# Kernel optimization log

Measured on AMD Instinct MI355X. Metric: run time of the kernel, lower is better.

The kernel has to match this reference:

```python
import jax, jax.numpy as jnp
import numpy as np

B, N1, N2, F = 8, 256, 256, 128


def setup_inputs() -> dict:
    key = jax.random.key(0)
    ks = jax.random.split(key, 12)
    s = 1.0 / np.sqrt(F)
    return {
        "x1": jax.random.normal(ks[0], (B, N1, F), jnp.float32),
        "x2": jax.random.normal(ks[1], (B, N2, F), jnp.float32),
        "valid_edge": (jax.random.uniform(ks[2], (B, N1, N2)) < 0.2).astype(jnp.float32),
        "W_w": jax.random.uniform(ks[3], (F, F), jnp.float32, -s, s),
        "W_b": jax.random.uniform(ks[4], (F,), jnp.float32, -s, s),
        "M_w": jax.random.uniform(ks[5], (F, F), jnp.float32, -s, s),
        "M_b": jax.random.uniform(ks[6], (F,), jnp.float32, -s, s),
        "gru_wih": jax.random.uniform(ks[7], (3 * F, F), jnp.float32, -s, s),
        "gru_whh": jax.random.uniform(ks[8], (3 * F, F), jnp.float32, -s, s),
        "gru_bih": jax.random.uniform(ks[9], (3 * F,), jnp.float32, -s, s),
        "gru_bhh": jax.random.uniform(ks[10], (3 * F,), jnp.float32, -s, s),
    }


def reference(x1, x2, valid_edge, W_w, W_b, M_w, M_b, gru_wih, gru_whh, gru_bih, gru_bhh):
    # m1 = W(x1)  [B,N1,F]
    m1 = jnp.einsum('bnf,gf->bng', x1, W_w) + W_b
    # Apply M once to x2 (equivalent to M on the repeated 4D tensor), then
    # masked max over neighbors j (N2): max_j( M(x2)[b,j,:] * mask[b,i,j] )
    Mx2 = jnp.einsum('bmf,gf->bmg', x2, M_w) + M_b          # [B,N2,F]
    masked = Mx2[:, None, :, :] * valid_edge[..., None]     # [B,N1,N2,F]
    m2 = jnp.max(masked, axis=2)                            # [B,N1,F]
    x = jax.nn.relu(m1 + m2)                                # GRU input
    # GRUCell(input=x, hidden=x1), torch semantics
    xf = x.reshape(-1, F)
    hf = x1.reshape(-1, F)
    gi = xf @ gru_wih.T + gru_bih                           # [B*N1, 3F]
    gh = hf @ gru_whh.T + gru_bhh
    ir, iz, in_ = jnp.split(gi, 3, axis=-1)
    hr, hz, hn = jnp.split(gh, 3, axis=-1)
    r = jax.nn.sigmoid(ir + hr)
    z = jax.nn.sigmoid(iz + hz)
    n = jnp.tanh(in_ + r * hn)
    h = (1.0 - z) * n + z * hf
    return h.reshape(B, N1, F)
```

## Files before the change

kernel.cpp:

```cpp
#include <hip/hip_runtime.h>


#define FDIM 128
#define N2DIM 256

__global__ __launch_bounds__(128)
void k_lin(const float* __restrict__ x1,
           const float* __restrict__ x2,
           const float* __restrict__ Ww,
           const float* __restrict__ Wb,
           const float* __restrict__ Mw,
           const float* __restrict__ Mb,
           float* __restrict__ m1, float* __restrict__ mx2)
{
  int blk = blockIdx.x;
  int which = blk >> 9;
  int row0 = (blk & 511) << 2;
  const float* X  = which ? x2 : x1;
  const float* W  = which ? Mw : Ww;
  const float* Bv = which ? Mb : Wb;
  float* out = which ? mx2 : m1;

  __shared__ float xs[4][FDIM];
  int tid = threadIdx.x;
#pragma unroll
  for (int r = 0; r < 4; ++r)
    xs[r][tid] = X[(size_t)(row0 + r) * FDIM + tid];
  __syncthreads();

  const float* wrow = W + (size_t)tid * FDIM;
  float acc[4] = {0.f,0.f,0.f,0.f};
  for (int k0 = 0; k0 < FDIM; k0 += 4) {
    float4 wv = *(const float4*)(wrow + k0);
#pragma unroll
    for (int r = 0; r < 4; ++r) {
      float4 xv = *(const float4*)(&xs[r][k0]);
      acc[r] += xv.x * wv.x + xv.y * wv.y + xv.z * wv.z + xv.w * wv.w;
    }
  }
  float bv = Bv[tid];
#pragma unroll
  for (int r = 0; r < 4; ++r)
    out[(size_t)(row0 + r) * FDIM + tid] = acc[r] + bv;
}

__global__ __launch_bounds__(128)
void k_maxrelu(const float* __restrict__ ve,
               const float* __restrict__ mx2,
               float* __restrict__ m1x)
{
  int blk = blockIdx.x;
  int b = blk >> 8;
  __shared__ int idx[N2DIM];
  __shared__ int cnt;
  __shared__ int nz;
  int tid = threadIdx.x;
  if (tid == 0) { cnt = 0; nz = 0; }
  __syncthreads();
  const float* e = ve + (size_t)blk * N2DIM;
  for (int j = tid; j < N2DIM; j += 128) {
    float v = e[j];
    if (v != 0.0f) { int p = atomicAdd(&cnt, 1); idx[p] = j; }
    else nz = 1;
  }
  __syncthreads();
  int n = cnt;
  const float* Mbase = mx2 + (size_t)b * N2DIM * FDIM + tid;
  float m2 = nz ? 0.0f : -3.0e38f;
  int i = 0;
  for (; i + 8 <= n; i += 8) {
    float v0 = Mbase[(size_t)idx[i]     * FDIM];
    float v1 = Mbase[(size_t)idx[i + 1] * FDIM];
    float v2 = Mbase[(size_t)idx[i + 2] * FDIM];
    float v3 = Mbase[(size_t)idx[i + 3] * FDIM];
    float v4 = Mbase[(size_t)idx[i + 4] * FDIM];
    float v5 = Mbase[(size_t)idx[i + 5] * FDIM];
    float v6 = Mbase[(size_t)idx[i + 6] * FDIM];
    float v7 = Mbase[(size_t)idx[i + 7] * FDIM];
    m2 = fmaxf(m2, fmaxf(fmaxf(fmaxf(v0, v1), fmaxf(v2, v3)),
                         fmaxf(fmaxf(v4, v5), fmaxf(v6, v7))));
  }
  for (; i < n; ++i)
    m2 = fmaxf(m2, Mbase[(size_t)idx[i] * FDIM]);
  size_t o = (size_t)blk * FDIM + tid;
  float s = m1x[o] + m2;
  m1x[o] = fmaxf(s, 0.0f);
}

__global__ __launch_bounds__(256)
void k_gru(const float* __restrict__ xw,
           const float* __restrict__ x1,
           const float* __restrict__ wih,
           const float* __restrict__ whh,
           const float* __restrict__ bih,
           const float* __restrict__ bhh,
           float* __restrict__ out)
{
  int row0 = blockIdx.x << 2;
  int tid = threadIdx.x;
  int f = tid & 127;
  int io = tid >> 7;

  __shared__ float tiles[2][4][FDIM];
  __shared__ float gh_sh[3][4][FDIM];

  for (int t = tid; t < 4 * FDIM; t += 256) {
    int r = t >> 7, c = t & 127;
    tiles[0][r][c] = xw[(size_t)(row0 + r) * FDIM + c];
    tiles[1][r][c] = x1[(size_t)(row0 + r) * FDIM + c];
  }
  __syncthreads();

  const float* Wm = io ? whh : wih;
  const float (*tile)[FDIM] = tiles[io];
  const float* w0p = Wm + (size_t)f * FDIM;
  const float* w1p = Wm + (size_t)(128 + f) * FDIM;
  const float* w2p = Wm + (size_t)(256 + f) * FDIM;

  float a0[4], a1[4], a2[4];
#pragma unroll
  for (int r = 0; r < 4; ++r) { a0[r] = 0.f; a1[r] = 0.f; a2[r] = 0.f; }

  for (int k0 = 0; k0 < FDIM; k0 += 4) {
    float4 c0 = *(const float4*)(w0p + k0);
    float4 c1 = *(const float4*)(w1p + k0);
    float4 c2 = *(const float4*)(w2p + k0);
#pragma unroll
    for (int r = 0; r < 4; ++r) {
      float4 tv = *(const float4*)(&tile[r][k0]);
      a0[r] += tv.x * c0.x + tv.y * c0.y + tv.z * c0.z + tv.w * c0.w;
      a1[r] += tv.x * c1.x + tv.y * c1.y + tv.z * c1.z + tv.w * c1.w;
      a2[r] += tv.x * c2.x + tv.y * c2.y + tv.z * c2.z + tv.w * c2.w;
    }
  }

  const float* Bv = io ? bhh : bih;
  float b0 = Bv[f], b1 = Bv[128 + f], b2 = Bv[256 + f];

  if (io) {
#pragma unroll
    for (int r = 0; r < 4; ++r) {
      gh_sh[0][r][f] = a0[r] + b0;
      gh_sh[1][r][f] = a1[r] + b1;
      gh_sh[2][r][f] = a2[r] + b2;
    }
  }
  __syncthreads();
  if (!io) {
#pragma unroll
    for (int r = 0; r < 4; ++r) {
      float ir  = a0[r] + b0, iz = a1[r] + b1, in_ = a2[r] + b2;
      float hr  = gh_sh[0][r][f];
      float hz  = gh_sh[1][r][f];
      float hn  = gh_sh[2][r][f];
      float rg  = 1.f / (1.f + __expf(-(ir + hr)));
      float zg  = 1.f / (1.f + __expf(-(iz + hz)));
      float pre = in_ + rg * hn;
      float e2  = __expf(2.f * pre);
      float nn  = 1.f - 2.f / (e2 + 1.f);
      float h   = (1.f - zg) * nn + zg * tiles[1][r][f];
      out[(size_t)(row0 + r) * FDIM + f] = h;
    }
  }
}

extern "C" void kernel_launch(void* const* d_in, const int* in_sizes, int n_in,
                              void* d_out, int out_size, void* d_ws, size_t ws_size,
                              hipStream_t stream) {
  (void)in_sizes; (void)n_in; (void)out_size; (void)ws_size;
  const float* x1  = (const float*)d_in[0];
  const float* x2  = (const float*)d_in[1];
  const float* ve  = (const float*)d_in[2];
  const float* Ww  = (const float*)d_in[3];
  const float* Wb  = (const float*)d_in[4];
  const float* Mw  = (const float*)d_in[5];
  const float* Mb  = (const float*)d_in[6];
  const float* wih = (const float*)d_in[7];
  const float* whh = (const float*)d_in[8];
  const float* bih = (const float*)d_in[9];
  const float* bhh = (const float*)d_in[10];
  float* out = (float*)d_out;

  float* ws  = (float*)d_ws;
  float* m1x = ws;
  float* mx2 = ws + 262144;

  hipLaunchKernelGGL(k_lin,     dim3(1024), dim3(128), 0, stream,
                     x1, x2, Ww, Wb, Mw, Mb, m1x, mx2);
  hipLaunchKernelGGL(k_maxrelu, dim3(2048), dim3(128), 0, stream,
                     ve, mx2, m1x);
  hipLaunchKernelGGL(k_gru,     dim3(512),  dim3(256), 0, stream,
                     m1x, x1, wih, whh, bih, bhh, out);
}
```

Measured before the change: 117.8 us.

## Fuse masked max-relu stage into GRU kernel, keeping GRU input in shared memory

```diff
diff --git a/kernel.cpp b/kernel.cpp
--- a/kernel.cpp
+++ b/kernel.cpp
@@ -44,75 +44,79 @@
     out[(size_t)(row0 + r) * FDIM + tid] = acc[r] + bv;
 }
 
-__global__ __launch_bounds__(128)
-void k_maxrelu(const float* __restrict__ ve,
-               const float* __restrict__ mx2,
-               float* __restrict__ m1x)
-{
-  int blk = blockIdx.x;
-  int b = blk >> 8;
-  __shared__ int idx[N2DIM];
-  __shared__ int cnt;
-  __shared__ int nz;
-  int tid = threadIdx.x;
-  if (tid == 0) { cnt = 0; nz = 0; }
-  __syncthreads();
-  const float* e = ve + (size_t)blk * N2DIM;
-  for (int j = tid; j < N2DIM; j += 128) {
-    float v = e[j];
-    if (v != 0.0f) { int p = atomicAdd(&cnt, 1); idx[p] = j; }
-    else nz = 1;
-  }
-  __syncthreads();
-  int n = cnt;
-  const float* Mbase = mx2 + (size_t)b * N2DIM * FDIM + tid;
-  float m2 = nz ? 0.0f : -3.0e38f;
-  int i = 0;
-  for (; i + 8 <= n; i += 8) {
-    float v0 = Mbase[(size_t)idx[i]     * FDIM];
-    float v1 = Mbase[(size_t)idx[i + 1] * FDIM];
-    float v2 = Mbase[(size_t)idx[i + 2] * FDIM];
-    float v3 = Mbase[(size_t)idx[i + 3] * FDIM];
-    float v4 = Mbase[(size_t)idx[i + 4] * FDIM];
-    float v5 = Mbase[(size_t)idx[i + 5] * FDIM];
-    float v6 = Mbase[(size_t)idx[i + 6] * FDIM];
-    float v7 = Mbase[(size_t)idx[i + 7] * FDIM];
-    m2 = fmaxf(m2, fmaxf(fmaxf(fmaxf(v0, v1), fmaxf(v2, v3)),
-                         fmaxf(fmaxf(v4, v5), fmaxf(v6, v7))));
-  }
-  for (; i < n; ++i)
-    m2 = fmaxf(m2, Mbase[(size_t)idx[i] * FDIM]);
-  size_t o = (size_t)blk * FDIM + tid;
-  float s = m1x[o] + m2;
-  m1x[o] = fmaxf(s, 0.0f);
-}
-
 __global__ __launch_bounds__(256)
-void k_gru(const float* __restrict__ xw,
-           const float* __restrict__ x1,
-           const float* __restrict__ wih,
-           const float* __restrict__ whh,
-           const float* __restrict__ bih,
-           const float* __restrict__ bhh,
-           float* __restrict__ out)
+void k_fused(const float* __restrict__ ve,
+             const float* __restrict__ mx2,
+             const float* __restrict__ m1,
+             const float* __restrict__ x1,
+             const float* __restrict__ wih,
+             const float* __restrict__ whh,
+             const float* __restrict__ bih,
+             const float* __restrict__ bhh,
+             float* __restrict__ out)
 {
   int row0 = blockIdx.x << 2;
+  int b = row0 >> 8;
   int tid = threadIdx.x;
-  int f = tid & 127;
-  int io = tid >> 7;
 
-  __shared__ float tiles[2][4][FDIM];
+  __shared__ float x_sh[4][FDIM];
+  __shared__ float h_sh[4][FDIM];
   __shared__ float gh_sh[3][4][FDIM];
+  __shared__ int idx[4][N2DIM];
+  __shared__ int cnt[4];
+  __shared__ int nz[4];
 
-  for (int t = tid; t < 4 * FDIM; t += 256) {
-    int r = t >> 7, c = t & 127;
-    tiles[0][r][c] = xw[(size_t)(row0 + r) * FDIM + c];
-    tiles[1][r][c] = x1[(size_t)(row0 + r) * FDIM + c];
+  for (int t = tid; t < 4 * FDIM; t += 256)
+    h_sh[t >> 7][t & 127] = x1[(size_t)row0 * FDIM + t];
+  if (tid < 4) { cnt[tid] = 0; nz[tid] = 0; }
+  __syncthreads();
+
+  {
+    int r = tid >> 6, l = tid & 63;
+    const float* e = ve + (size_t)(row0 + r) * N2DIM;
+#pragma unroll
+    for (int j0 = 0; j0 < N2DIM; j0 += 64) {
+      float v = e[j0 + l];
+      if (v != 0.0f) { int p = atomicAdd(&cnt[r], 1); idx[r][p] = j0 + l; }
+      else nz[r] = 1;
+    }
   }
   __syncthreads();
 
+  {
+    int half = tid >> 7, f = tid & 127;
+    const float* Mbase = mx2 + (size_t)b * N2DIM * FDIM + f;
+#pragma unroll
+    for (int rr = 0; rr < 2; ++rr) {
+      int r = half + (rr << 1);
+      int n = cnt[r];
+      const int* ix = idx[r];
+      float m2 = nz[r] ? 0.0f : -3.0e38f;
+      int i = 0;
+      for (; i + 8 <= n; i += 8) {
+        float v0 = Mbase[(size_t)ix[i]     * FDIM];
+        float v1 = Mbase[(size_t)ix[i + 1] * FDIM];
+        float v2 = Mbase[(size_t)ix[i + 2] * FDIM];
+        float v3 = Mbase[(size_t)ix[i + 3] * FDIM];
+        float v4 = Mbase[(size_t)ix[i + 4] * FDIM];
+        float v5 = Mbase[(size_t)ix[i + 5] * FDIM];
+        float v6 = Mbase[(size_t)ix[i + 6] * FDIM];
+        float v7 = Mbase[(size_t)ix[i + 7] * FDIM];
+        m2 = fmaxf(m2, fmaxf(fmaxf(fmaxf(v0, v1), fmaxf(v2, v3)),
+                             fmaxf(fmaxf(v4, v5), fmaxf(v6, v7))));
+      }
+      for (; i < n; ++i)
+        m2 = fmaxf(m2, Mbase[(size_t)ix[i] * FDIM]);
+      float s = m1[(size_t)(row0 + r) * FDIM + f] + m2;
+      x_sh[r][f] = fmaxf(s, 0.0f);
+    }
+  }
+  __syncthreads();
+
+  int f = tid & 127;
+  int io = tid >> 7;
   const float* Wm = io ? whh : wih;
-  const float (*tile)[FDIM] = tiles[io];
+  const float (*tile)[FDIM] = io ? h_sh : x_sh;
   const float* w0p = Wm + (size_t)f * FDIM;
   const float* w1p = Wm + (size_t)(128 + f) * FDIM;
   const float* w2p = Wm + (size_t)(256 + f) * FDIM;
@@ -158,7 +162,7 @@
       float pre = in_ + rg * hn;
       float e2  = __expf(2.f * pre);
       float nn  = 1.f - 2.f / (e2 + 1.f);
-      float h   = (1.f - zg) * nn + zg * tiles[1][r][f];
+      float h   = (1.f - zg) * nn + zg * h_sh[r][f];
       out[(size_t)(row0 + r) * FDIM + f] = h;
     }
   }
@@ -182,13 +186,11 @@
   float* out = (float*)d_out;
 
   float* ws  = (float*)d_ws;
-  float* m1x = ws;
+  float* m1  = ws;
   float* mx2 = ws + 262144;
 
-  hipLaunchKernelGGL(k_lin,     dim3(1024), dim3(128), 0, stream,
-                     x1, x2, Ww, Wb, Mw, Mb, m1x, mx2);
-  hipLaunchKernelGGL(k_maxrelu, dim3(2048), dim3(128), 0, stream,
-                     ve, mx2, m1x);
-  hipLaunchKernelGGL(k_gru,     dim3(512),  dim3(256), 0, stream,
-                     m1x, x1, wih, whh, bih, bhh, out);
+  hipLaunchKernelGGL(k_lin,   dim3(1024), dim3(128), 0, stream,
+                     x1, x2, Ww, Wb, Mw, Mb, m1, mx2);
+  hipLaunchKernelGGL(k_fused, dim3(512),  dim3(256), 0, stream,
+                     ve, mx2, m1, x1, wih, whh, bih, bhh, out);
 }
```

After: 117.7 us. About the same (-0.1%).
